# Performance work log

Hardware: AMD Instinct MI355X
Metric: run time of the kernel (lower is better)

## Reference

```python
import jax, jax.numpy as jnp
import numpy as np

N, IN_DIM, E_DIM, H, D = 10000, 128, 32, 4, 32
NE = 640000
OUT_DIM = D  # out Linear maps H*D -> out_dim == D here (32)


def setup_inputs() -> dict:
    key = jax.random.key(0)
    ks = jax.random.split(key, 12)
    HD = H * D
    s = lambda k, sh, fan: jax.random.normal(k, sh, jnp.float32) / np.sqrt(fan)
    return {
        "x": jax.random.normal(ks[0], (N, IN_DIM), jnp.float32),
        "edge_index": jax.random.randint(ks[1], (2, NE), 0, N),
        "edge_attr": jax.random.normal(ks[2], (NE, E_DIM), jnp.float32),
        "Wq": s(ks[3], (IN_DIM, HD), IN_DIM), "bq": jnp.zeros((HD,), jnp.float32),
        "Wk": s(ks[4], (IN_DIM, HD), IN_DIM), "bk": jnp.zeros((HD,), jnp.float32),
        "Wv": s(ks[5], (IN_DIM, HD), IN_DIM), "bv": jnp.zeros((HD,), jnp.float32),
        "We": s(ks[6], (E_DIM, HD), E_DIM), "be": jnp.zeros((HD,), jnp.float32),
        "Wo": s(ks[7], (HD, OUT_DIM), HD), "bo": jnp.zeros((OUT_DIM,), jnp.float32),
    }


def reference(x, edge_index, edge_attr, Wq, bq, Wk, bk, Wv, bv, We, be, Wo, bo):
    n = x.shape[0]
    Q = (x @ Wq + bq).reshape(-1, H, D)
    K = (x @ Wk + bk).reshape(-1, H, D)
    V = (x @ Wv + bv).reshape(-1, H, D)
    Ef = (edge_attr @ We + be).reshape(-1, H, D)
    src, dst = edge_index[0], edge_index[1]
    # per-edge scores [E, H]: QK dot over src/dst gather + E self dot
    scores = (jnp.einsum('ehd,ehd->eh', Q[src], K[dst])
              + jnp.einsum('ehd,ehd->eh', Ef, Ef)) / np.sqrt(D).astype(np.float32)
    alpha = jax.nn.softmax(scores, axis=-1)  # softmax over heads (as in source)
    out_e = (alpha[..., None] * V[dst]).reshape(-1, H * D)  # [E, H*D]
    out_e = out_e @ Wo + bo  # [E, out_dim]
    # scatter-mean by source node
    sums = jax.ops.segment_sum(out_e, src, num_segments=n)
    cnt = jax.ops.segment_sum(jnp.ones((out_e.shape[0],), out_e.dtype), src, num_segments=n)
    return sums / jnp.maximum(cnt, 1.0)[:, None]
```

## Files before the change

kernel.cpp:

```cpp
#include <hip/hip_runtime.h>

#define NN      10000
#define IN_DIM  128
#define E_DIM   32
#define NH      4
#define DH      32
#define HD      128
#define NE_     640000
#define OUT_DIM 32
#define SCAN_T  1024
#define CHUNK   10
#define NTILES  (NN / 16)
#define NTASKS  (NTILES * 3)
#define QKVP_BLKS  469
#define HIST_BLKS  (NE_ / 256)
#define EE_BLKS    (NE_ / 256)

typedef __attribute__((ext_vector_type(8))) short bf16x8;
typedef __attribute__((ext_vector_type(4))) float f32x4;

static __device__ __forceinline__ unsigned short f32_to_bf16_rne(float f) {
    unsigned u = __float_as_uint(f);
    return (unsigned short)((u + 0x7fffu + ((u >> 16) & 1u)) >> 16);
}
static __device__ __forceinline__ float bf16_bits_to_f32(unsigned short h) {
    return __uint_as_float(((unsigned)h) << 16);
}
static __device__ __forceinline__ float blo(unsigned u) { return __uint_as_float(u << 16); }
static __device__ __forceinline__ float bhi(unsigned u) { return __uint_as_float(u & 0xffff0000u); }

__global__ __launch_bounds__(256) void prep_kernel(
    const float* __restrict__ Wq, const float* __restrict__ Wk,
    const float* __restrict__ Wv, const float* __restrict__ Wo,
    const float* __restrict__ bv, const float* __restrict__ We,
    const int*   __restrict__ ei,
    unsigned short* __restrict__ wfh, unsigned short* __restrict__ wfl,
    unsigned short* __restrict__ wefh, unsigned short* __restrict__ wefl,
    float* __restrict__ bp,
    int* __restrict__ deg, int* __restrict__ rank)
{
    const int blk = blockIdx.x;
    const int t = threadIdx.x;

    if (blk < 24) {
        const int tid = blk * 256 + t;
        const int l = tid & 63;
        const int ts = tid >> 6;
        const int s = ts & 3, tt = ts >> 2;
        const int col = (tt & 7) * 16 + (l & 15);
        if (tt < 16) {
            const float* __restrict__ W = (tt < 8) ? Wq : Wk;
            #pragma unroll
            for (int j = 0; j < 8; ++j) {
                const int k = s * 32 + (l >> 4) * 8 + j;
                const float w = W[k * HD + col];
                const unsigned short hi = f32_to_bf16_rne(w);
                wfh[tid * 8 + j] = hi;
                wfl[tid * 8 + j] = f32_to_bf16_rne(w - bf16_bits_to_f32(hi));
            }
        } else {
            const int h = col & 3, oo = col >> 2;
            #pragma unroll
            for (int j = 0; j < 8; ++j) {
                const int k = s * 32 + (l >> 4) * 8 + j;
                float acc = 0.f;
                #pragma unroll
                for (int d2 = 0; d2 < DH; ++d2)
                    acc = fmaf(Wv[k * HD + h * DH + d2],
                               Wo[(h * DH + d2) * OUT_DIM + oo], acc);
                const unsigned short hi = f32_to_bf16_rne(acc);
                wfh[tid * 8 + j] = hi;
                wfl[tid * 8 + j] = f32_to_bf16_rne(acc - bf16_bits_to_f32(hi));
            }
        }
    } else if (blk < 26) {
        const int tid = (blk - 24) * 256 + t;
        const int l = tid & 63, tt = tid >> 6;
        #pragma unroll
        for (int j = 0; j < 8; ++j) {
            const int k = (l >> 4) * 8 + j;
            const int d = tt * 16 + (l & 15);
            const float w = We[k * HD + d];
            const unsigned short hi = f32_to_bf16_rne(w);
            wefh[tid * 8 + j] = hi;
            wefl[tid * 8 + j] = f32_to_bf16_rne(w - bf16_bits_to_f32(hi));
        }
    } else if (blk == 26) {
        if (t < HD) {
            const int h = t & 3, oo = t >> 2;
            float b = 0.f;
            #pragma unroll
            for (int d2 = 0; d2 < DH; ++d2)
                b = fmaf(bv[h * DH + d2], Wo[(h * DH + d2) * OUT_DIM + oo], b);
            bp[t] = b;
        }
    } else {
        const int e = (blk - 27) * 256 + t;
        rank[e] = atomicAdd(&deg[ei[e]], 1);
    }
}

__global__ __launch_bounds__(SCAN_T) void scan_kernel(
    const int* __restrict__ deg, int* __restrict__ off)
{
    __shared__ int wsum[16];
    const int t = threadIdx.x;
    const int lane = t & 63, w = t >> 6;
    const int base = t * CHUNK;
    int v[CHUNK];
    int sum = 0;
    #pragma unroll
    for (int i = 0; i < CHUNK; ++i) {
        const int idx = base + i;
        v[i] = (idx < NN) ? deg[idx] : 0;
        sum += v[i];
    }
    int incl = sum;
    #pragma unroll
    for (int dlt = 1; dlt < 64; dlt <<= 1) {
        const int nb = __shfl_up(incl, dlt, 64);
        if (lane >= dlt) incl += nb;
    }
    if (lane == 63) wsum[w] = incl;
    __syncthreads();
    if (w == 0) {
        const int val = (lane < 16) ? wsum[lane] : 0;
        int wi = val;
        #pragma unroll
        for (int dlt = 1; dlt < 16; dlt <<= 1) {
            const int nb = __shfl_up(wi, dlt, 64);
            if (lane >= dlt) wi += nb;
        }
        if (lane < 16) wsum[lane] = wi - val;
    }
    __syncthreads();
    int run = wsum[w] + (incl - sum);
    #pragma unroll
    for (int i = 0; i < CHUNK; ++i) {
        const int idx = base + i;
        if (idx < NN) { off[idx] = run; run += v[i]; }
    }
}

__global__ __launch_bounds__(256) void mm_kernel(
    const float* __restrict__ x,
    const unsigned short* __restrict__ wfh, const unsigned short* __restrict__ wfl,
    const float* __restrict__ bq, const float* __restrict__ bk,
    const float* __restrict__ bp,
    float* __restrict__ Q, unsigned short* __restrict__ KPTb,
    const float* __restrict__ ea,
    const unsigned short* __restrict__ wefh, const unsigned short* __restrict__ wefl,
    const float* __restrict__ be,
    const int* __restrict__ ei,
    const int* __restrict__ off, const int* __restrict__ rank,
    float4* __restrict__ eev, int* __restrict__ ids)
{
    const int lane = threadIdx.x & 63;
    const int wave = threadIdx.x >> 6;

    if (blockIdx.x < QKVP_BLKS) {
        const int task = blockIdx.x * 4 + wave;
        if (task >= NTASKS) return;
        const int nt = task / 3, cg = task - nt * 3;
        const int node = nt * 16 + (lane & 15);
        const int kc = lane >> 4;

        bf16x8 xh0, xl0, xh1, xl1, xh2, xl2, xh3, xl3;
#define SPL(VH, VL, I, VAL) { \
    const unsigned short hh = f32_to_bf16_rne(VAL); \
    VH[I] = (short)hh; VL[I] = (short)f32_to_bf16_rne((VAL) - bf16_bits_to_f32(hh)); }
#define LOAD_X(S, VH, VL) { \
    const float* xr = x + (size_t)node * IN_DIM + (S) * 32 + kc * 8; \
    const float4 a0 = *reinterpret_cast<const float4*>(xr); \
    const float4 a1 = *reinterpret_cast<const float4*>(xr + 4); \
    SPL(VH, VL, 0, a0.x) SPL(VH, VL, 1, a0.y) SPL(VH, VL, 2, a0.z) SPL(VH, VL, 3, a0.w) \
    SPL(VH, VL, 4, a1.x) SPL(VH, VL, 5, a1.y) SPL(VH, VL, 6, a1.z) SPL(VH, VL, 7, a1.w) }
        LOAD_X(0, xh0, xl0) LOAD_X(1, xh1, xl1) LOAD_X(2, xh2, xl2) LOAD_X(3, xh3, xl3)
#undef LOAD_X
#undef SPL

        const float* __restrict__ bb = (cg == 0) ? bq : (cg == 1) ? bk : bp;

#define KSTEP(S, FB, FB2, XH, XL) { \
    const bf16x8 wh = *reinterpret_cast<const bf16x8*>((FB)  + (S) * 64 * 8); \
    const bf16x8 wl = *reinterpret_cast<const bf16x8*>((FB2) + (S) * 64 * 8); \
    acc = __builtin_amdgcn_mfma_f32_16x16x32_bf16(wh, XH, acc, 0, 0, 0); \
    acc = __builtin_amdgcn_mfma_f32_16x16x32_bf16(wh, XL, acc, 0, 0, 0); \
    acc = __builtin_amdgcn_mfma_f32_16x16x32_bf16(wl, XH, acc, 0, 0, 0); }

#define TILE(TLOC) { \
    const unsigned short* fb  = wfh + ((((cg * 8 + TLOC) * 4) * 64 + lane) << 3); \
    const unsigned short* fb2 = wfl + ((((cg * 8 + TLOC) * 4) * 64 + lane) << 3); \
    const float4 b4 = *reinterpret_cast<const float4*>(bb + (TLOC) * 16 + (kc << 2)); \
    f32x4 acc = {b4.x, b4.y, b4.z, b4.w}; \
    KSTEP(0, fb, fb2, xh0, xl0) KSTEP(1, fb, fb2, xh1, xl1) \
    KSTEP(2, fb, fb2, xh2, xl2) KSTEP(3, fb, fb2, xh3, xl3) \
    const int j0 = (TLOC) * 16 + (kc << 2); \
    if (cg == 0) { \
        *reinterpret_cast<float4*>(Q + (size_t)node * HD + j0) = \
            make_float4(acc[0], acc[1], acc[2], acc[3]); \
    } else { \
        unsigned short* dp = KPTb + (size_t)node * 256 + j0 * 2 + ((cg == 1) ? 0 : 4); \
        *reinterpret_cast<ushort4*>(dp) = make_ushort4( \
            f32_to_bf16_rne(acc[0]), f32_to_bf16_rne(acc[1]), \
            f32_to_bf16_rne(acc[2]), f32_to_bf16_rne(acc[3])); \
    } }

        TILE(0) TILE(1) TILE(2) TILE(3) TILE(4) TILE(5) TILE(6) TILE(7)
#undef TILE
#undef KSTEP
        return;
    }

    const int base = (blockIdx.x - QKVP_BLKS) * 256 + wave * 64;

    const int src  = ei[base + lane];
    const int dstn = ei[NE_ + base + lane];
    const int pos  = off[src] + rank[base + lane];

    const int erow = lane & 15;
    const int kc = lane >> 4;
    bf16x8 ah0, ah1, ah2, ah3;
#define LOAD_A(AT, VAR) { \
    const float* ar = ea + (size_t)(base + AT * 16 + erow) * E_DIM + kc * 8; \
    const float4 a0 = *reinterpret_cast<const float4*>(ar); \
    const float4 a1 = *reinterpret_cast<const float4*>(ar + 4); \
    VAR[0] = (short)f32_to_bf16_rne(a0.x); VAR[1] = (short)f32_to_bf16_rne(a0.y); \
    VAR[2] = (short)f32_to_bf16_rne(a0.z); VAR[3] = (short)f32_to_bf16_rne(a0.w); \
    VAR[4] = (short)f32_to_bf16_rne(a1.x); VAR[5] = (short)f32_to_bf16_rne(a1.y); \
    VAR[6] = (short)f32_to_bf16_rne(a1.z); VAR[7] = (short)f32_to_bf16_rne(a1.w); }
    LOAD_A(0, ah0) LOAD_A(1, ah1) LOAD_A(2, ah2) LOAD_A(3, ah3)
#undef LOAD_A

    float p00 = 0.f, p01 = 0.f, p02 = 0.f, p03 = 0.f;
    float p10 = 0.f, p11 = 0.f, p12 = 0.f, p13 = 0.f;
    float p20 = 0.f, p21 = 0.f, p22 = 0.f, p23 = 0.f;
    float p30 = 0.f, p31 = 0.f, p32 = 0.f, p33 = 0.f;

#define AT_BODY(AT, H, WHI, WLO, BE4) { \
    f32x4 acc = {BE4.x, BE4.y, BE4.z, BE4.w}; \
    acc = __builtin_amdgcn_mfma_f32_16x16x32_bf16(WLO, ah##AT, acc, 0, 0, 0); \
    acc = __builtin_amdgcn_mfma_f32_16x16x32_bf16(WHI, ah##AT, acc, 0, 0, 0); \
    p##AT##H = fmaf(acc[0], acc[0], fmaf(acc[1], acc[1], \
               fmaf(acc[2], acc[2], fmaf(acc[3], acc[3], p##AT##H)))); }

#define TILE(T, H) { \
    const bf16x8 whi = *reinterpret_cast<const bf16x8*>(wefh + ((T * 64 + lane) << 3)); \
    const bf16x8 wlo = *reinterpret_cast<const bf16x8*>(wefl + ((T * 64 + lane) << 3)); \
    const float4 be4 = *reinterpret_cast<const float4*>(be + T * 16 + ((lane >> 4) << 2)); \
    AT_BODY(0, H, whi, wlo, be4) AT_BODY(1, H, whi, wlo, be4) \
    AT_BODY(2, H, whi, wlo, be4) AT_BODY(3, H, whi, wlo, be4) }

    TILE(0, 0) TILE(1, 0) TILE(2, 1) TILE(3, 1)
    TILE(4, 2) TILE(5, 2) TILE(6, 3) TILE(7, 3)
#undef TILE
#undef AT_BODY

#define RED(AT, H) \
    float r##AT##H = p##AT##H; \
    r##AT##H += __shfl_xor(r##AT##H, 16, 64); \
    r##AT##H += __shfl_xor(r##AT##H, 32, 64);
    RED(0, 0) RED(0, 1) RED(0, 2) RED(0, 3)
    RED(1, 0) RED(1, 1) RED(1, 2) RED(1, 3)
    RED(2, 0) RED(2, 1) RED(2, 2) RED(2, 3)
    RED(3, 0) RED(3, 1) RED(3, 2) RED(3, 3)
#undef RED

    const int at4 = lane >> 4;
#define SEL(H) ((at4 & 2) ? ((at4 & 1) ? r3##H : r2##H) : ((at4 & 1) ? r1##H : r0##H))
    const float w0 = SEL(0), w1 = SEL(1), w2 = SEL(2), w3 = SEL(3);
#undef SEL

    eev[base + lane] = make_float4(__int_as_float(dstn), w0 - w3, w1 - w3, w2 - w3);
    ids[pos] = base + lane;
}

__global__ __launch_bounds__(256) void fused_gather_kernel(
    const int* __restrict__ off, const int* __restrict__ deg,
    const int* __restrict__ ids, const float4* __restrict__ eev,
    const float* __restrict__ Q, const unsigned short* __restrict__ KPTb,
    const float* __restrict__ bo, float* __restrict__ out)
{
    __shared__ float red[16][OUT_DIM];
    const int n = blockIdx.x;
    const int d = deg[n];
    const int start = off[n];
    const int tid = threadIdx.x;
    const int g = tid >> 4;
    const int o16 = tid & 15;
    const int h = o16 >> 2;
    const float scale = 0.17677669529663687f;

    const float* __restrict__ qrow = Q + (size_t)n * HD + o16 * 8;
    const float4 qa = *reinterpret_cast<const float4*>(qrow);
    const float4 qb = *reinterpret_cast<const float4*>(qrow + 4);

    float acc0 = 0.f, acc1 = 0.f;

    float4 pc = make_float4(0.f, 0.f, 0.f, 0.f);
    int idn = 0;
    if (g < d)      pc  = eev[ids[start + g]];
    if (g + 16 < d) idn = ids[start + g + 16];

    for (int i = g; i < d; i += 16) {
        int idn2 = 0;
        if (i + 32 < d) idn2 = ids[start + i + 32];
        float4 pn = make_float4(0.f, 0.f, 0.f, 0.f);
        if (i + 16 < d) pn = eev[idn];

        const int dst = __float_as_int(pc.x);
        const unsigned short* __restrict__ kp = KPTb + (size_t)dst * 256 + o16 * 16;
        const uint4 u0 = *reinterpret_cast<const uint4*>(kp);
        const uint4 u1 = *reinterpret_cast<const uint4*>(kp + 8);

        float p =           qa.x * blo(u0.x);
        p = fmaf(qa.y, bhi(u0.x), p);
        p = fmaf(qa.z, blo(u0.y), p);
        p = fmaf(qa.w, bhi(u0.y), p);
        p = fmaf(qb.x, blo(u1.x), p);
        p = fmaf(qb.y, bhi(u1.x), p);
        p = fmaf(qb.z, blo(u1.y), p);
        p = fmaf(qb.w, bhi(u1.y), p);
        p += __shfl_xor(p, 1, 64);
        p += __shfl_xor(p, 2, 64);
        const float b  = __shfl_xor(p, 4, 64);
        const float e0 = (h & 1) ? b : p;
        const float e1 = (h & 1) ? p : b;
        const float o0 = __shfl_xor(e0, 8, 64);
        const float o1 = __shfl_xor(e1, 8, 64);
        const float qk0 = (h & 2) ? o0 : e0;
        const float qk1 = (h & 2) ? o1 : e1;
        const float qk2 = (h & 2) ? e0 : o0;
        const float qk3 = (h & 2) ? e1 : o1;

        const float s0 = (qk0 + pc.y) * scale;
        const float s1 = (qk1 + pc.z) * scale;
        const float s2 = (qk2 + pc.w) * scale;
        const float s3 = qk3 * scale;
        const float mx = fmaxf(fmaxf(s0, s1), fmaxf(s2, s3));
        const float a0 = __expf(s0 - mx), a1 = __expf(s1 - mx);
        const float a2 = __expf(s2 - mx), a3 = __expf(s3 - mx);
        const float inv = 1.f / (a0 + a1 + a2 + a3);

        float c0 =          a0 * blo(u0.z);
        c0 = fmaf(a1, bhi(u0.z), c0);
        c0 = fmaf(a2, blo(u0.w), c0);
        c0 = fmaf(a3, bhi(u0.w), c0);
        float c1 =          a0 * blo(u1.z);
        c1 = fmaf(a1, bhi(u1.z), c1);
        c1 = fmaf(a2, blo(u1.w), c1);
        c1 = fmaf(a3, bhi(u1.w), c1);
        acc0 = fmaf(c0, inv, acc0);
        acc1 = fmaf(c1, inv, acc1);

        pc = pn; idn = idn2;
    }
    red[g][o16 * 2]     = acc0;
    red[g][o16 * 2 + 1] = acc1;
    __syncthreads();
    if (tid < 32) {
        float s = 0.f;
        #pragma unroll
        for (int gg = 0; gg < 16; ++gg) s += red[gg][tid];
        out[(size_t)n * OUT_DIM + tid] = (d > 0) ? (s / (float)d + bo[tid]) : 0.f;
    }
}

extern "C" void kernel_launch(void* const* d_in, const int* in_sizes, int n_in,
                              void* d_out, int out_size, void* d_ws, size_t ws_size,
                              hipStream_t stream)
{
    const float* x   = (const float*)d_in[0];
    const int*   ei  = (const int*)  d_in[1];
    const float* ea  = (const float*)d_in[2];
    const float* Wq  = (const float*)d_in[3];
    const float* bq  = (const float*)d_in[4];
    const float* Wk  = (const float*)d_in[5];
    const float* bk  = (const float*)d_in[6];
    const float* Wv  = (const float*)d_in[7];
    const float* bv  = (const float*)d_in[8];
    const float* We  = (const float*)d_in[9];
    const float* be  = (const float*)d_in[10];
    const float* Wo  = (const float*)d_in[11];
    const float* bo  = (const float*)d_in[12];
    float* out = (float*)d_out;

    float*  Q    = (float*)d_ws;
    float4* eev  = (float4*)(Q + (size_t)NN * HD);
    unsigned short* KPTb = (unsigned short*)(eev + NE_);
    float*  bp   = (float*)(KPTb + (size_t)NN * 256);
    unsigned short* wefh = (unsigned short*)(bp + HD);
    unsigned short* wefl = wefh + 8 * 64 * 8;
    unsigned short* wfh  = wefl + 8 * 64 * 8;
    unsigned short* wfl  = wfh + 24 * 4 * 64 * 8;
    int* rank = (int*)(wfl + 24 * 4 * 64 * 8);
    int* ids  = rank + NE_;
    int* deg  = ids + NE_;
    int* off  = deg + NN;

    hipMemsetAsync(deg, 0, NN * sizeof(int), stream);

    prep_kernel<<<27 + HIST_BLKS, 256, 0, stream>>>(Wq, Wk, Wv, Wo, bv, We, ei,
                                                    wfh, wfl, wefh, wefl, bp,
                                                    deg, rank);
    scan_kernel<<<1, SCAN_T, 0, stream>>>(deg, off);
    mm_kernel<<<QKVP_BLKS + EE_BLKS, 256, 0, stream>>>(x, wfh, wfl, bq, bk, bp,
                                                       Q, KPTb, ea, wefh, wefl,
                                                       be, ei, off, rank, eev, ids);
    fused_gather_kernel<<<NN, 256, 0, stream>>>(off, deg, ids, eev, Q, KPTb, bo, out);
}
```

Before: 127.9 us.

## Split ids scatter into separate blocks and stage edge_attr through LDS

The ids scatter (off[src]+rank) moves out of the edge-embedding blocks into its own set of blocks at the front of the mm_kernel grid. The edge blocks now load their 64x32 edge_attr tile with fully coalesced float4 reads into padded shared memory, then build the MFMA operands from LDS instead of strided global loads. This targets uncoalesced global access and the dependent gather chain in the edge path. In exchange it adds about 36 KB of shared memory to every block, including the QKV blocks that never use it, which can lower occupancy, and it adds a block-wide barrier.

```diff
diff --git a/kernel.cpp b/kernel.cpp
--- a/kernel.cpp
+++ b/kernel.cpp
@@ -12,9 +12,10 @@
 #define CHUNK   10
 #define NTILES  (NN / 16)
 #define NTASKS  (NTILES * 3)
+#define IDS_BLKS   (NE_ / 256)
 #define QKVP_BLKS  469
+#define EE_BLKS    (NE_ / 256)
 #define HIST_BLKS  (NE_ / 256)
-#define EE_BLKS    (NE_ / 256)
 
 typedef __attribute__((ext_vector_type(8))) short bf16x8;
 typedef __attribute__((ext_vector_type(4))) float f32x4;
@@ -155,11 +156,18 @@
     const int* __restrict__ off, const int* __restrict__ rank,
     float4* __restrict__ eev, int* __restrict__ ids)
 {
+    __shared__ float eas[4][64][36];
     const int lane = threadIdx.x & 63;
     const int wave = threadIdx.x >> 6;
 
-    if (blockIdx.x < QKVP_BLKS) {
-        const int task = blockIdx.x * 4 + wave;
+    if (blockIdx.x < IDS_BLKS) {
+        const int e = blockIdx.x * 256 + threadIdx.x;
+        ids[off[ei[e]] + rank[e]] = e;
+        return;
+    }
+
+    if (blockIdx.x < IDS_BLKS + QKVP_BLKS) {
+        const int task = (blockIdx.x - IDS_BLKS) * 4 + wave;
         if (task >= NTASKS) return;
         const int nt = task / 3, cg = task - nt * 3;
         const int node = nt * 16 + (lane & 15);
@@ -212,17 +220,27 @@
         return;
     }
 
-    const int base = (blockIdx.x - QKVP_BLKS) * 256 + wave * 64;
-
-    const int src  = ei[base + lane];
+    const int base = (blockIdx.x - IDS_BLKS - QKVP_BLKS) * 256 + wave * 64;
+
+    {
+        const float4* __restrict__ gsrc =
+            reinterpret_cast<const float4*>(ea + (size_t)base * E_DIM);
+        #pragma unroll
+        for (int r = 0; r < 8; ++r) {
+            const int idx = r * 64 + lane;
+            const float4 v = gsrc[idx];
+            *reinterpret_cast<float4*>(&eas[wave][idx >> 3][(idx & 7) * 4]) = v;
+        }
+    }
+    __syncthreads();
+
     const int dstn = ei[NE_ + base + lane];
-    const int pos  = off[src] + rank[base + lane];
 
     const int erow = lane & 15;
     const int kc = lane >> 4;
     bf16x8 ah0, ah1, ah2, ah3;
 #define LOAD_A(AT, VAR) { \
-    const float* ar = ea + (size_t)(base + AT * 16 + erow) * E_DIM + kc * 8; \
+    const float* ar = &eas[wave][AT * 16 + erow][kc * 8]; \
     const float4 a0 = *reinterpret_cast<const float4*>(ar); \
     const float4 a1 = *reinterpret_cast<const float4*>(ar + 4); \
     VAR[0] = (short)f32_to_bf16_rne(a0.x); VAR[1] = (short)f32_to_bf16_rne(a0.y); \
@@ -272,7 +290,6 @@
 #undef SEL
 
     eev[base + lane] = make_float4(__int_as_float(dstn), w0 - w3, w1 - w3, w2 - w3);
-    ids[pos] = base + lane;
 }
 
 __global__ __launch_bounds__(256) void fused_gather_kernel(
@@ -404,8 +421,8 @@
                                                     wfh, wfl, wefh, wefl, bp,
                                                     deg, rank);
     scan_kernel<<<1, SCAN_T, 0, stream>>>(deg, off);
-    mm_kernel<<<QKVP_BLKS + EE_BLKS, 256, 0, stream>>>(x, wfh, wfl, bq, bk, bp,
-                                                       Q, KPTb, ea, wefh, wefl,
-                                                       be, ei, off, rank, eev, ids);
+    mm_kernel<<<IDS_BLKS + QKVP_BLKS + EE_BLKS, 256, 0, stream>>>(
+        x, wfh, wfl, bq, bk, bp, Q, KPTb, ea, wefh, wefl, be, ei, off, rank,
+        eev, ids);
     fused_gather_kernel<<<NN, 256, 0, stream>>>(off, deg, ids, eev, Q, KPTb, bo, out);
 }
```

New measurement: 129.0 us. Within noise of the previous version (+0.9%).

## Scatter edge payload directly to CSR order and prefetch next K rows

Applied to the files above, without the earlier changes.

The edge-score kernel now writes each edge's float4 payload (dst index plus score differences) straight into its sorted CSR position, instead of writing it in edge order alongside a separate id permutation. The gather kernel therefore reads the payload contiguously with no extra indirection through the ids array. The gather loop also software-pipelines the dependent K/V row load one iteration ahead, so that the dst-indexed gather overlaps with compute. In exchange the writes become scattered, and keeping the prefetched rows live uses more registers.

```diff
diff --git a/kernel.cpp b/kernel.cpp
--- a/kernel.cpp
+++ b/kernel.cpp
@@ -13,8 +13,8 @@
 #define NTILES  (NN / 16)
 #define NTASKS  (NTILES * 3)
 #define QKVP_BLKS  469
+#define EE_BLKS    (NE_ / 256)
 #define HIST_BLKS  (NE_ / 256)
-#define EE_BLKS    (NE_ / 256)
 
 typedef __attribute__((ext_vector_type(8))) short bf16x8;
 typedef __attribute__((ext_vector_type(4))) float f32x4;
@@ -153,7 +153,7 @@
     const float* __restrict__ be,
     const int* __restrict__ ei,
     const int* __restrict__ off, const int* __restrict__ rank,
-    float4* __restrict__ eev, int* __restrict__ ids)
+    float4* __restrict__ pay)
 {
     const int lane = threadIdx.x & 63;
     const int wave = threadIdx.x >> 6;
@@ -271,13 +271,12 @@
     const float w0 = SEL(0), w1 = SEL(1), w2 = SEL(2), w3 = SEL(3);
 #undef SEL
 
-    eev[base + lane] = make_float4(__int_as_float(dstn), w0 - w3, w1 - w3, w2 - w3);
-    ids[pos] = base + lane;
+    pay[pos] = make_float4(__int_as_float(dstn), w0 - w3, w1 - w3, w2 - w3);
 }
 
 __global__ __launch_bounds__(256) void fused_gather_kernel(
     const int* __restrict__ off, const int* __restrict__ deg,
-    const int* __restrict__ ids, const float4* __restrict__ eev,
+    const float4* __restrict__ pay,
     const float* __restrict__ Q, const unsigned short* __restrict__ KPTb,
     const float* __restrict__ bo, float* __restrict__ out)
 {
@@ -298,29 +297,36 @@
     float acc0 = 0.f, acc1 = 0.f;
 
     float4 pc = make_float4(0.f, 0.f, 0.f, 0.f);
-    int idn = 0;
-    if (g < d)      pc  = eev[ids[start + g]];
-    if (g + 16 < d) idn = ids[start + g + 16];
+    float4 pn = make_float4(0.f, 0.f, 0.f, 0.f);
+    if (g < d)      pc = pay[start + g];
+    if (g + 16 < d) pn = pay[start + g + 16];
+    uint4 uc0, uc1;
+    {
+        const unsigned short* __restrict__ kp =
+            KPTb + (size_t)__float_as_int(pc.x) * 256 + o16 * 16;
+        uc0 = *reinterpret_cast<const uint4*>(kp);
+        uc1 = *reinterpret_cast<const uint4*>(kp + 8);
+    }
 
     for (int i = g; i < d; i += 16) {
-        int idn2 = 0;
-        if (i + 32 < d) idn2 = ids[start + i + 32];
-        float4 pn = make_float4(0.f, 0.f, 0.f, 0.f);
-        if (i + 16 < d) pn = eev[idn];
-
-        const int dst = __float_as_int(pc.x);
-        const unsigned short* __restrict__ kp = KPTb + (size_t)dst * 256 + o16 * 16;
-        const uint4 u0 = *reinterpret_cast<const uint4*>(kp);
-        const uint4 u1 = *reinterpret_cast<const uint4*>(kp + 8);
-
-        float p =           qa.x * blo(u0.x);
-        p = fmaf(qa.y, bhi(u0.x), p);
-        p = fmaf(qa.z, blo(u0.y), p);
-        p = fmaf(qa.w, bhi(u0.y), p);
-        p = fmaf(qb.x, blo(u1.x), p);
-        p = fmaf(qb.y, bhi(u1.x), p);
-        p = fmaf(qb.z, blo(u1.y), p);
-        p = fmaf(qb.w, bhi(u1.y), p);
+        float4 pn2 = make_float4(0.f, 0.f, 0.f, 0.f);
+        if (i + 32 < d) pn2 = pay[start + i + 32];
+        uint4 un0 = make_uint4(0, 0, 0, 0), un1 = make_uint4(0, 0, 0, 0);
+        if (i + 16 < d) {
+            const unsigned short* __restrict__ kp =
+                KPTb + (size_t)__float_as_int(pn.x) * 256 + o16 * 16;
+            un0 = *reinterpret_cast<const uint4*>(kp);
+            un1 = *reinterpret_cast<const uint4*>(kp + 8);
+        }
+
+        float p =           qa.x * blo(uc0.x);
+        p = fmaf(qa.y, bhi(uc0.x), p);
+        p = fmaf(qa.z, blo(uc0.y), p);
+        p = fmaf(qa.w, bhi(uc0.y), p);
+        p = fmaf(qb.x, blo(uc1.x), p);
+        p = fmaf(qb.y, bhi(uc1.x), p);
+        p = fmaf(qb.z, blo(uc1.y), p);
+        p = fmaf(qb.w, bhi(uc1.y), p);
         p += __shfl_xor(p, 1, 64);
         p += __shfl_xor(p, 2, 64);
         const float b  = __shfl_xor(p, 4, 64);
@@ -342,18 +348,18 @@
         const float a2 = __expf(s2 - mx), a3 = __expf(s3 - mx);
         const float inv = 1.f / (a0 + a1 + a2 + a3);
 
-        float c0 =          a0 * blo(u0.z);
-        c0 = fmaf(a1, bhi(u0.z), c0);
-        c0 = fmaf(a2, blo(u0.w), c0);
-        c0 = fmaf(a3, bhi(u0.w), c0);
-        float c1 =          a0 * blo(u1.z);
-        c1 = fmaf(a1, bhi(u1.z), c1);
-        c1 = fmaf(a2, blo(u1.w), c1);
-        c1 = fmaf(a3, bhi(u1.w), c1);
+        float c0 =          a0 * blo(uc0.z);
+        c0 = fmaf(a1, bhi(uc0.z), c0);
+        c0 = fmaf(a2, blo(uc0.w), c0);
+        c0 = fmaf(a3, bhi(uc0.w), c0);
+        float c1 =          a0 * blo(uc1.z);
+        c1 = fmaf(a1, bhi(uc1.z), c1);
+        c1 = fmaf(a2, blo(uc1.w), c1);
+        c1 = fmaf(a3, bhi(uc1.w), c1);
         acc0 = fmaf(c0, inv, acc0);
         acc1 = fmaf(c1, inv, acc1);
 
-        pc = pn; idn = idn2;
+        pc = pn; pn = pn2; uc0 = un0; uc1 = un1;
     }
     red[g][o16 * 2]     = acc0;
     red[g][o16 * 2 + 1] = acc1;
@@ -386,16 +392,15 @@
     float* out = (float*)d_out;
 
     float*  Q    = (float*)d_ws;
-    float4* eev  = (float4*)(Q + (size_t)NN * HD);
-    unsigned short* KPTb = (unsigned short*)(eev + NE_);
+    float4* pay  = (float4*)(Q + (size_t)NN * HD);
+    unsigned short* KPTb = (unsigned short*)(pay + NE_);
     float*  bp   = (float*)(KPTb + (size_t)NN * 256);
     unsigned short* wefh = (unsigned short*)(bp + HD);
     unsigned short* wefl = wefh + 8 * 64 * 8;
     unsigned short* wfh  = wefl + 8 * 64 * 8;
     unsigned short* wfl  = wfh + 24 * 4 * 64 * 8;
     int* rank = (int*)(wfl + 24 * 4 * 64 * 8);
-    int* ids  = rank + NE_;
-    int* deg  = ids + NE_;
+    int* deg  = rank + NE_;
     int* off  = deg + NN;
 
     hipMemsetAsync(deg, 0, NN * sizeof(int), stream);
@@ -406,6 +411,6 @@
     scan_kernel<<<1, SCAN_T, 0, stream>>>(deg, off);
     mm_kernel<<<QKVP_BLKS + EE_BLKS, 256, 0, stream>>>(x, wfh, wfl, bq, bk, bp,
                                                        Q, KPTb, ea, wefh, wefl,
-                                                       be, ei, off, rank, eev, ids);
-    fused_gather_kernel<<<NN, 256, 0, stream>>>(off, deg, ids, eev, Q, KPTb, bo, out);
-}
+                                                       be, ei, off, rank, pay);
+    fused_gather_kernel<<<NN, 256, 0, stream>>>(off, deg, pay, Q, KPTb, bo, out);
+}
```

Measured after the change: 124.6 us. 2.6% less time.
